# Kernel optimization log

Measured on AMD Instinct MI355X. Metric: run time of the kernel, lower is better.

Reference implementation:

```python
import jax, jax.numpy as jnp
import numpy as np

B, L, H, F, K, NBINS, T = 32, 512, 512, 512, 3, 256, 4096
EPS = 1e-8  # RMSNorm epsilon
PAD = (K - 1) // 2  # =1, matches both conv paddings in the torch module


def _conv1d(x, w, b):
    # x: [B, L, Cin], w: [K, Cin, Cout]
    return jax.lax.conv_general_dilated(
        x, w, window_strides=(1,), padding=[(PAD, PAD)],
        dimension_numbers=('NLC', 'LIO', 'NLC')) + b


def _rms(x, g):
    return g * x / (jnp.sqrt(jnp.mean(x * x, axis=-1, keepdims=True)) + EPS)


def _vpred(x, mask, w1, b1, g1, w2, b2, g2, wl, bl):
    h = _rms(jax.nn.relu(_conv1d(x, w1, b1)), g1)
    h = _rms(jax.nn.relu(_conv1d(h, w2, b2)), g2)
    out = (h @ wl + bl)[..., 0]  # [B, L]
    return jnp.where(mask, 0.0, out)


def _proj(x, w1, b1, w2, b2):
    return jax.nn.relu(jax.nn.relu(x @ w1 + b1) @ w2 + b2)


def _length_regulate(x, dur, max_len):
    # Vectorized equivalent of LengthRegulator: repeat phoneme i dur[b,i] times, pad to max_len.
    cum = jnp.cumsum(dur, axis=1)               # [B, L]
    mel_len = cum[:, -1]                        # [B]
    t = jnp.arange(max_len)                     # [T]
    idx = jax.vmap(lambda c: jnp.searchsorted(c, t, side='right'))(cum)  # [B, T]
    idx = jnp.minimum(idx, x.shape[1] - 1)
    out = jnp.take_along_axis(x, idx[:, :, None], axis=1)  # [B, T, H]
    valid = (t[None, :] < mel_len[:, None])
    return out * valid[:, :, None].astype(x.dtype), mel_len


def setup_inputs() -> dict:
    key = jax.random.key(0)
    ks = iter(jax.random.split(key, 64))
    n = lambda *s: jax.random.normal(next(ks), s, jnp.float32) * 0.05
    inp = {}
    inp['x'] = jax.random.normal(next(ks), (B, L, H), jnp.float32)
    inp['embedding'] = jax.random.normal(next(ks), (B, L, H), jnp.float32)
    inp['src_mask'] = jnp.zeros((B, L), bool)
    inp['duration_target'] = jax.random.randint(next(ks), (B, L), 0, 9, jnp.int32)
    inp['pitch_target'] = jax.random.normal(next(ks), (B, L), jnp.float32)
    inp['energy_target'] = jax.random.normal(next(ks), (B, L), jnp.float32)
    inp['max_len'] = T
    for p in ['dur', 'pit', 'eng']:
        inp[p + '_w1'] = n(K, H, F); inp[p + '_b1'] = jnp.zeros(F, jnp.float32)
        inp[p + '_g1'] = jnp.ones(F, jnp.float32)
        inp[p + '_w2'] = n(K, F, F); inp[p + '_b2'] = jnp.zeros(F, jnp.float32)
        inp[p + '_g2'] = jnp.ones(F, jnp.float32)
        inp[p + '_wl'] = n(F, 1); inp[p + '_bl'] = jnp.zeros(1, jnp.float32)
    for p in ['pp', 'ep', 'sp']:
        inp[p + '_w1'] = n(H, H); inp[p + '_b1'] = jnp.zeros(H, jnp.float32)
        inp[p + '_w2'] = n(H, H); inp[p + '_b2'] = jnp.zeros(H, jnp.float32)
    inp['pitch_bins'] = jnp.linspace(-3.0, 3.0, NBINS - 1)
    inp['energy_bins'] = jnp.linspace(-3.0, 3.0, NBINS - 1)
    inp['pitch_emb'] = n(NBINS, H)
    inp['energy_emb'] = n(NBINS, H)
    return inp


def reference(x, embedding, src_mask, duration_target, pitch_target, energy_target, max_len,
              dur_w1, dur_b1, dur_g1, dur_w2, dur_b2, dur_g2, dur_wl, dur_bl,
              pit_w1, pit_b1, pit_g1, pit_w2, pit_b2, pit_g2, pit_wl, pit_bl,
              eng_w1, eng_b1, eng_g1, eng_w2, eng_b2, eng_g2, eng_wl, eng_bl,
              pp_w1, pp_b1, pp_w2, pp_b2,
              ep_w1, ep_b1, ep_w2, ep_b2,
              sp_w1, sp_b1, sp_w2, sp_b2,
              pitch_bins, energy_bins, pitch_emb, energy_emb):
    log_dur = _vpred(x, src_mask, dur_w1, dur_b1, dur_g1, dur_w2, dur_b2, dur_g2, dur_wl, dur_bl)
    pit_pred = _vpred(x + _proj(embedding, pp_w1, pp_b1, pp_w2, pp_b2), src_mask,
                      pit_w1, pit_b1, pit_g1, pit_w2, pit_b2, pit_g2, pit_wl, pit_bl)
    pitch_embedding = pitch_emb[jnp.searchsorted(pitch_bins, pitch_target)]  # torch.bucketize right=False == side='left'
    eng_pred = _vpred(x + _proj(embedding, ep_w1, ep_b1, ep_w2, ep_b2), src_mask,
                      eng_w1, eng_b1, eng_g1, eng_w2, eng_b2, eng_g2, eng_wl, eng_bl)
    energy_embedding = energy_emb[jnp.searchsorted(energy_bins, energy_target)]
    xo = x + energy_embedding + pitch_embedding + _proj(embedding, sp_w1, sp_b1, sp_w2, sp_b2)
    out, mel_len = _length_regulate(xo, duration_target, max_len)
    return (out, pit_pred, eng_pred, log_dur, mel_len)
```

## Files before the change

### kernel.cpp

```cpp
#include <hip/hip_runtime.h>

#define Bv    32
#define Lv    512
#define Hv    512
#define Fv    512
#define Tv    4096
#define Mv    (Bv*Lv)
#define NBINSv 256

#define OUT_OFF 0
#define PIT_OFF (Bv*(size_t)Tv*Hv)
#define ENG_OFF (PIT_OFF + Mv)
#define DUR_OFF (ENG_OFF + Mv)
#define MEL_OFF (DUR_OFF + Mv)

typedef unsigned short ushort;
typedef __attribute__((ext_vector_type(8))) short   bf16x8;
typedef __attribute__((ext_vector_type(4))) float   f32x4;
typedef __attribute__((ext_vector_type(8))) unsigned short u16x8;

__device__ __forceinline__ float b2f(ushort u) {
    union { float f; unsigned u; } x; x.u = ((unsigned)u) << 16; return x.f;
}
__device__ __forceinline__ ushort f2b(float f) {
    union { float f; unsigned u; } x; x.f = f;
    unsigned r = x.u + 0x7fffu + ((x.u >> 16) & 1u);
    return (ushort)(r >> 16);
}

#define GLL16(g, l) __builtin_amdgcn_global_load_lds( \
    (const __attribute__((address_space(1))) void*)(g), \
    (__attribute__((address_space(3))) void*)(l), 16, 0, 0)

template<int NZ> struct GArgs {
    const ushort* A[NZ];
    const ushort* W[NZ];
    const float*  bias[NZ];
    ushort*       C[NZ];
};
struct RmsArgs   { const ushort* h[3]; const float* g[3]; ushort* o[3]; };
struct RlArgs    { const ushort* h[3]; const float* g[3]; const float* wl[3]; const float* bl[3]; };
struct TransArgs { const float* src[6]; ushort* dst[6]; };
struct ConvArgs  { const float* src[2]; ushort* dst[2]; };

template<int NTAPS, int EPI, int NZ>
__global__ __launch_bounds__(256) void gemm_bf16_kernel(
    GArgs<NZ> ga, const float* __restrict__ res, const float* __restrict__ pe,
    const float* __restrict__ ee, const int* __restrict__ idxp,
    const int* __restrict__ idxe, const ushort* __restrict__ zp)
{
    constexpr int KTOT = NTAPS * 512;
    const int z = (NZ > 1) ? blockIdx.z : 0;
    const ushort* __restrict__ A    = ga.A[z];
    const ushort* __restrict__ Bt   = ga.W[z];
    const float*  __restrict__ bias = ga.bias[z];
    ushort*       __restrict__ C    = ga.C[z];

    __shared__ ushort As[128 * 32];
    __shared__ ushort Bs[128 * 32];

    const int tid = threadIdx.x;
    const int n0 = blockIdx.x * 128;
    const int m0 = blockIdx.y * 128;

    const int sar = tid >> 2;
    const int sl  = tid & 3;

    const int lane = tid & 63;
    const int w    = tid >> 6;
    const int wm   = (w & 1) * 64;
    const int wn   = (w >> 1) * 64;
    const int lr   = lane & 15;
    const int q    = lane >> 4;

    ushort* asd0 = &As[sar * 32 + sl * 8];
    ushort* asd1 = &As[(sar + 64) * 32 + sl * 8];
    ushort* bsd0 = &Bs[sar * 32 + sl * 8];
    ushort* bsd1 = &Bs[(sar + 64) * 32 + sl * 8];

    f32x4 acc[4][4];
    #pragma unroll
    for (int j = 0; j < 4; ++j)
        #pragma unroll
        for (int i = 0; i < 4; ++i) {
            f32x4 zz = {0.f, 0.f, 0.f, 0.f};
            acc[j][i] = zz;
        }

    for (int tap = 0; tap < NTAPS; ++tap) {
        const ushort* ab[2];
        #pragma unroll
        for (int r = 0; r < 2; ++r) {
            const int row = sar + r * 64;
            const int m   = m0 + row;
            if (NTAPS == 3) {
                const int l  = m & (Lv - 1);
                const int ls = l + tap - 1;
                ab[r] = ((unsigned)ls < (unsigned)Lv)
                      ? A + (size_t)(m + tap - 1) * 512 + sl * 8 : nullptr;
            } else {
                ab[r] = A + (size_t)m * 512 + sl * 8;
            }
        }
        const ushort* bb0 = Bt + (size_t)(n0 + sar) * KTOT + tap * 512 + sl * 8;
        const ushort* bb1 = Bt + (size_t)(n0 + sar + 64) * KTOT + tap * 512 + sl * 8;

        for (int kt = 0; kt < 16; ++kt) {
            const int kin = kt << 5;
            GLL16(ab[0] ? ab[0] + kin : zp, asd0);
            GLL16(bb0 + kin, bsd0);
            GLL16(ab[1] ? ab[1] + kin : zp, asd1);
            GLL16(bb1 + kin, bsd1);
            __syncthreads();

            bf16x8 af[4], bfr[4];
            #pragma unroll
            for (int i = 0; i < 4; ++i) {
                af[i]  = *(const bf16x8*)&As[(wm + i * 16 + lr) * 32 + q * 8];
                bfr[i] = *(const bf16x8*)&Bs[(wn + i * 16 + lr) * 32 + q * 8];
            }
            #pragma unroll
            for (int j = 0; j < 4; ++j)
                #pragma unroll
                for (int i = 0; i < 4; ++i)
                    acc[j][i] = __builtin_amdgcn_mfma_f32_16x16x32_bf16(
                                    bfr[j], af[i], acc[j][i], 0, 0, 0);
            __syncthreads();
        }
    }

    #pragma unroll
    for (int i = 0; i < 4; ++i) {
        const int m = m0 + wm + i * 16 + lr;
        const size_t ro = (size_t)m * 512;
        int ip = 0, ie = 0;
        if (EPI == 2) { ip = idxp[m]; ie = idxe[m]; }
        #pragma unroll
        for (int j = 0; j < 4; ++j) {
            const int n = n0 + wn + j * 16 + q * 4;
            const f32x4 a = acc[j][i];
            const float4 bi = *(const float4*)(bias + n);
            float v0 = fmaxf(a[0] + bi.x, 0.f);
            float v1 = fmaxf(a[1] + bi.y, 0.f);
            float v2 = fmaxf(a[2] + bi.z, 0.f);
            float v3 = fmaxf(a[3] + bi.w, 0.f);
            if (EPI >= 1) {
                const float4 r4 = *(const float4*)(res + ro + n);
                v0 += r4.x; v1 += r4.y; v2 += r4.z; v3 += r4.w;
            }
            if (EPI == 2) {
                const float4 p4 = *(const float4*)(pe + (size_t)ip * 512 + n);
                const float4 e4 = *(const float4*)(ee + (size_t)ie * 512 + n);
                v0 += p4.x + e4.x; v1 += p4.y + e4.y;
                v2 += p4.z + e4.z; v3 += p4.w + e4.w;
            }
            ushort4 o4;
            o4.x = f2b(v0); o4.y = f2b(v1); o4.z = f2b(v2); o4.w = f2b(v3);
            *(ushort4*)(C + ro + n) = o4;
        }
    }
}

__global__ __launch_bounds__(256) void convert_kernel(ConvArgs ca)
{
    const float* __restrict__ X  = ca.src[blockIdx.y];
    ushort*      __restrict__ Xb = ca.dst[blockIdx.y];
    const size_t i = (size_t)blockIdx.x * 256 + threadIdx.x;
    const float4 a = ((const float4*)X)[2 * i];
    const float4 b = ((const float4*)X)[2 * i + 1];
    u16x8 o;
    o[0] = f2b(a.x); o[1] = f2b(a.y); o[2] = f2b(a.z); o[3] = f2b(a.w);
    o[4] = f2b(b.x); o[5] = f2b(b.y); o[6] = f2b(b.z); o[7] = f2b(b.w);
    *(u16x8*)(Xb + i * 8) = o;
}

__global__ __launch_bounds__(256) void transpose_kernel(TransArgs ta, int Ktot)
{
    const float* __restrict__ W  = ta.src[blockIdx.z];
    ushort*      __restrict__ Wt = ta.dst[blockIdx.z];
    __shared__ float t[32][33];
    const int k0 = blockIdx.x * 32, n0 = blockIdx.y * 32;
    const int r = threadIdx.x >> 5, c = threadIdx.x & 31;
    #pragma unroll
    for (int rr = 0; rr < 4; ++rr)
        t[r + rr * 8][c] = W[(size_t)(k0 + r + rr * 8) * 512 + n0 + c];
    __syncthreads();
    #pragma unroll
    for (int rr = 0; rr < 4; ++rr)
        Wt[(size_t)(n0 + r + rr * 8) * Ktot + k0 + c] = f2b(t[c][r + rr * 8]);
}

__global__ __launch_bounds__(128) void rms_kernel(RmsArgs ra)
{
    const int z = blockIdx.y;
    const int row = blockIdx.x;
    const int tid = threadIdx.x;
    const ushort* __restrict__ h = ra.h[z];
    const ushort4 hv = ((const ushort4*)(h + (size_t)row * 512))[tid];
    const float v0 = b2f(hv.x), v1 = b2f(hv.y), v2 = b2f(hv.z), v3 = b2f(hv.w);
    float ss = v0 * v0 + v1 * v1 + v2 * v2 + v3 * v3;
    #pragma unroll
    for (int off = 32; off; off >>= 1) ss += __shfl_down(ss, off, 64);
    __shared__ float p[2];
    if ((tid & 63) == 0) p[tid >> 6] = ss;
    __syncthreads();
    const float tot = p[0] + p[1];
    const float inv = 1.f / (sqrtf(tot * (1.f / 512.f)) + 1e-8f);
    const float4 gv = ((const float4*)ra.g[z])[tid];
    ushort4 ov;
    ov.x = f2b(gv.x * v0 * inv); ov.y = f2b(gv.y * v1 * inv);
    ov.z = f2b(gv.z * v2 * inv); ov.w = f2b(gv.w * v3 * inv);
    ((ushort4*)(ra.o[z] + (size_t)row * 512))[tid] = ov;
}

__global__ __launch_bounds__(256) void rmslin_kernel(
    RlArgs ra, const unsigned char* __restrict__ mask, float* __restrict__ predbase)
{
    const int z = blockIdx.y;
    const int wave = threadIdx.x >> 6, lane = threadIdx.x & 63;
    const int row = blockIdx.x * 4 + wave;
    const ushort* __restrict__ h = ra.h[z];
    const bf16x8 hv = *(const bf16x8*)(h + (size_t)row * 512 + lane * 8);
    const float4 g0 = *(const float4*)(ra.g[z] + lane * 8);
    const float4 g1 = *(const float4*)(ra.g[z] + lane * 8 + 4);
    const float4 w0 = *(const float4*)(ra.wl[z] + lane * 8);
    const float4 w1 = *(const float4*)(ra.wl[z] + lane * 8 + 4);
    float hf[8];
    #pragma unroll
    for (int t = 0; t < 8; ++t) hf[t] = b2f((ushort)hv[t]);
    float ss = 0.f, sgw = 0.f;
    #pragma unroll
    for (int t = 0; t < 8; ++t) ss += hf[t] * hf[t];
    sgw += hf[0]*g0.x*w0.x + hf[1]*g0.y*w0.y + hf[2]*g0.z*w0.z + hf[3]*g0.w*w0.w;
    sgw += hf[4]*g1.x*w1.x + hf[5]*g1.y*w1.y + hf[6]*g1.z*w1.z + hf[7]*g1.w*w1.w;
    #pragma unroll
    for (int off = 32; off; off >>= 1) {
        ss  += __shfl_down(ss,  off, 64);
        sgw += __shfl_down(sgw, off, 64);
    }
    if (lane == 0) {
        const float inv = 1.f / (sqrtf(ss * (1.f / 512.f)) + 1e-8f);
        predbase[(size_t)z * Mv + row] = mask[row] ? 0.f : (sgw * inv + ra.bl[z][0]);
    }
}

__global__ __launch_bounds__(256) void idx_kernel(
    const float* __restrict__ pt, const float* __restrict__ et,
    const float* __restrict__ pbins, const float* __restrict__ ebins,
    int* __restrict__ idxp, int* __restrict__ idxe)
{
    __shared__ float pb[NBINSv - 1], ebn[NBINSv - 1];
    const int tid = threadIdx.x;
    if (tid < NBINSv - 1) { pb[tid] = pbins[tid]; ebn[tid] = ebins[tid]; }
    __syncthreads();
    const int m = blockIdx.x * 256 + tid;
    const float pv = pt[m], ev = et[m];
    int lo = 0, hi = NBINSv - 1;
    while (lo < hi) { int mid = (lo + hi) >> 1; if (pb[mid] < pv) lo = mid + 1; else hi = mid; }
    idxp[m] = lo;
    lo = 0; hi = NBINSv - 1;
    while (lo < hi) { int mid = (lo + hi) >> 1; if (ebn[mid] < ev) lo = mid + 1; else hi = mid; }
    idxe[m] = lo;
}

__global__ __launch_bounds__(512) void cumtmap_kernel(
    const int* __restrict__ dur, float* __restrict__ melout, int* __restrict__ tmap)
{
    __shared__ int s[Lv];
    const int b = blockIdx.x, tid = threadIdx.x;
    s[tid] = dur[b * Lv + tid];
    __syncthreads();
    for (int off = 1; off < Lv; off <<= 1) {
        int t = (tid >= off) ? s[tid - off] : 0;
        __syncthreads();
        s[tid] += t;
        __syncthreads();
    }
    const int mel = s[Lv - 1];
    if (tid == 0) melout[b] = (float)mel;
    #pragma unroll
    for (int rr = 0; rr < Tv / 512; ++rr) {
        const int t = tid + rr * 512;
        int lo = 0, hi = Lv;
        while (lo < hi) { int mid = (lo + hi) >> 1; if (s[mid] <= t) lo = mid + 1; else hi = mid; }
        tmap[b * Tv + t] = (t < mel) ? (b * Lv + min(lo, Lv - 1)) : -1;
    }
}

__global__ __launch_bounds__(128) void regulate_kernel(
    const ushort* __restrict__ xo, const int* __restrict__ tmap,
    float* __restrict__ out)
{
    const int bt = blockIdx.x;
    const int src = tmap[bt];
    float4 v = make_float4(0.f, 0.f, 0.f, 0.f);
    if (src >= 0) {
        const ushort4 u = ((const ushort4*)(xo + (size_t)src * 512))[threadIdx.x];
        v.x = b2f(u.x); v.y = b2f(u.y); v.z = b2f(u.z); v.w = b2f(u.w);
    }
    ((float4*)(out + (size_t)bt * 512))[threadIdx.x] = v;
}

extern "C" void kernel_launch(void* const* d_in, const int* in_sizes, int n_in,
                              void* d_out, int out_size, void* d_ws, size_t ws_size,
                              hipStream_t stream)
{
    const float* x    = (const float*)d_in[0];
    const float* emb  = (const float*)d_in[1];
    const unsigned char* mask = (const unsigned char*)d_in[2];
    const int*   durt = (const int*)d_in[3];
    const float* pt   = (const float*)d_in[4];
    const float* et   = (const float*)d_in[5];
    const float* dw1 = (const float*)d_in[7],  *db1 = (const float*)d_in[8],
               * dg1 = (const float*)d_in[9],  *dw2 = (const float*)d_in[10],
               * db2 = (const float*)d_in[11], *dg2 = (const float*)d_in[12],
               * dwl = (const float*)d_in[13], *dbl = (const float*)d_in[14];
    const float* pw1 = (const float*)d_in[15], *pb1 = (const float*)d_in[16],
               * pg1 = (const float*)d_in[17], *pw2 = (const float*)d_in[18],
               * pb2 = (const float*)d_in[19], *pg2 = (const float*)d_in[20],
               * pwl = (const float*)d_in[21], *pbl = (const float*)d_in[22];
    const float* ew1 = (const float*)d_in[23], *eb1 = (const float*)d_in[24],
               * eg1 = (const float*)d_in[25], *ew2 = (const float*)d_in[26],
               * eb2 = (const float*)d_in[27], *eg2 = (const float*)d_in[28],
               * ewl = (const float*)d_in[29], *ebl = (const float*)d_in[30];
    const float* ppw1 = (const float*)d_in[31], *ppb1 = (const float*)d_in[32],
               * ppw2 = (const float*)d_in[33], *ppb2 = (const float*)d_in[34];
    const float* epw1 = (const float*)d_in[35], *epb1 = (const float*)d_in[36],
               * epw2 = (const float*)d_in[37], *epb2 = (const float*)d_in[38];
    const float* spw1 = (const float*)d_in[39], *spb1 = (const float*)d_in[40],
               * spw2 = (const float*)d_in[41], *spb2 = (const float*)d_in[42];
    const float* pbins = (const float*)d_in[43];
    const float* ebins = (const float*)d_in[44];
    const float* pemb  = (const float*)d_in[45];
    const float* eemb  = (const float*)d_in[46];

    float* outf = (float*)d_out;

    int*    idxp   = (int*)d_ws;
    int*    idxe   = idxp + 16384;
    ushort* zp     = (ushort*)(idxe + 16384);
    int*    tmap   = idxe + 16448;
    ushort* xob    = (ushort*)((float*)d_ws + 262144);

    #define OBUF(i) ((ushort*)(outf + (size_t)(i) * 4194304))
    ushort* xb  = OBUF(0);   ushort* eb  = OBUF(1);
    ushort* pA0 = OBUF(2);   ushort* pA1 = OBUF(3);  ushort* pA2 = OBUF(4);
    ushort* xp  = OBUF(5);   ushort* xe  = OBUF(6);
    ushort* c0  = OBUF(7);   ushort* c1  = OBUF(8);  ushort* c2  = OBUF(9);
    ushort* r0  = OBUF(10);  ushort* r1  = OBUF(11); ushort* r2  = OBUF(12);
    ushort* wt[12];
    {
        size_t off = 13ull * 4194304;
        for (int i = 0; i < 6; ++i)  { wt[i] = (ushort*)(outf + off); off += 393216; }
        for (int i = 6; i < 12; ++i) { wt[i] = (ushort*)(outf + off); off += 131072; }
    }

    hipMemsetAsync(zp, 0, 64, stream);

    { ConvArgs ca = {{x, emb}, {xb, eb}};
      convert_kernel<<<dim3(4096, 2), 256, 0, stream>>>(ca); }
    { TransArgs ta = {{dw1, dw2, pw1, pw2, ew1, ew2}, {wt[0], wt[1], wt[2], wt[3], wt[4], wt[5]}};
      transpose_kernel<<<dim3(48, 16, 6), 256, 0, stream>>>(ta, 1536); }
    { TransArgs ta = {{ppw1, ppw2, epw1, epw2, spw1, spw2},
                      {wt[6], wt[7], wt[8], wt[9], wt[10], wt[11]}};
      transpose_kernel<<<dim3(16, 16, 6), 256, 0, stream>>>(ta, 512); }

    idx_kernel<<<Mv / 256, 256, 0, stream>>>(pt, et, pbins, ebins, idxp, idxe);
    cumtmap_kernel<<<Bv, Lv, 0, stream>>>(durt, outf + MEL_OFF, tmap);

    const dim3 g3(Fv / 128, Mv / 128, 3);
    const dim3 g2(Fv / 128, Mv / 128, 2);
    const dim3 g1(Fv / 128, Mv / 128, 1);

    { GArgs<3> a = {{eb, eb, eb}, {wt[6], wt[8], wt[10]}, {ppb1, epb1, spb1}, {pA0, pA1, pA2}};
      gemm_bf16_kernel<1, 0, 3><<<g3, 256, 0, stream>>>(a, nullptr, nullptr, nullptr,
                                                        nullptr, nullptr, zp); }
    { GArgs<2> a = {{pA0, pA1}, {wt[7], wt[9]}, {ppb2, epb2}, {xp, xe}};
      gemm_bf16_kernel<1, 1, 2><<<g2, 256, 0, stream>>>(a, x, nullptr, nullptr,
                                                        nullptr, nullptr, zp); }
    { GArgs<1> a = {{pA2}, {wt[11]}, {spb2}, {xob}};
      gemm_bf16_kernel<1, 2, 1><<<g1, 256, 0, stream>>>(a, x, pemb, eemb, idxp, idxe, zp); }

    { GArgs<3> a = {{xp, xe, xb}, {wt[2], wt[4], wt[0]}, {pb1, eb1, db1}, {c0, c1, c2}};
      gemm_bf16_kernel<3, 0, 3><<<g3, 256, 0, stream>>>(a, nullptr, nullptr, nullptr,
                                                        nullptr, nullptr, zp); }
    { RmsArgs ra = {{c0, c1, c2}, {pg1, eg1, dg1}, {r0, r1, r2}};
      rms_kernel<<<dim3(Mv, 3), 128, 0, stream>>>(ra); }
    { GArgs<3> a = {{r0, r1, r2}, {wt[3], wt[5], wt[1]}, {pb2, eb2, db2}, {c0, c1, c2}};
      gemm_bf16_kernel<3, 0, 3><<<g3, 256, 0, stream>>>(a, nullptr, nullptr, nullptr,
                                                        nullptr, nullptr, zp); }
    { RlArgs ra = {{c0, c1, c2}, {pg2, eg2, dg2}, {pwl, ewl, dwl}, {pbl, ebl, dbl}};
      rmslin_kernel<<<dim3(Mv / 4, 3), 256, 0, stream>>>(ra, mask, outf + PIT_OFF); }

    regulate_kernel<<<Bv * Tv, 128, 0, stream>>>(xob, tmap, outf + OUT_OFF);
}
```

Measured before the change: 880.7 us.

## Double-buffer GEMM LDS tiles, swizzle LDS layout, merge second projection GEMMs

The bf16 GEMM now double-buffers its A/B tiles in shared memory. The load for the next k-step is issued before computing the current one, with a single barrier per iteration, and the tap loop is flattened into one k loop. The LDS column chunks are rotated by row (a swizzle on both the global-load source and the fragment read) to reduce bank conflicts. The epilogue mode becomes a per-z runtime field, so the two second-stage projection GEMMs (EPI 1 and EPI 2) merge into one 3-way launch. In exchange, shared memory per block doubles and the epilogue carries runtime branches.

Result: no change. 868.9 us (-1.3%).

```diff
diff --git a/kernel.cpp b/kernel.cpp
--- a/kernel.cpp
+++ b/kernel.cpp
@@ -37,27 +37,30 @@
     const ushort* W[NZ];
     const float*  bias[NZ];
     ushort*       C[NZ];
+    int           epi[NZ];
 };
 struct RmsArgs   { const ushort* h[3]; const float* g[3]; ushort* o[3]; };
 struct RlArgs    { const ushort* h[3]; const float* g[3]; const float* wl[3]; const float* bl[3]; };
 struct TransArgs { const float* src[6]; ushort* dst[6]; };
 struct ConvArgs  { const float* src[2]; ushort* dst[2]; };
 
-template<int NTAPS, int EPI, int NZ>
+template<int NTAPS, int NZ>
 __global__ __launch_bounds__(256) void gemm_bf16_kernel(
     GArgs<NZ> ga, const float* __restrict__ res, const float* __restrict__ pe,
     const float* __restrict__ ee, const int* __restrict__ idxp,
     const int* __restrict__ idxe, const ushort* __restrict__ zp)
 {
     constexpr int KTOT = NTAPS * 512;
+    constexpr int KT   = NTAPS * 16;
     const int z = (NZ > 1) ? blockIdx.z : 0;
     const ushort* __restrict__ A    = ga.A[z];
     const ushort* __restrict__ Bt   = ga.W[z];
     const float*  __restrict__ bias = ga.bias[z];
     ushort*       __restrict__ C    = ga.C[z];
-
-    __shared__ ushort As[128 * 32];
-    __shared__ ushort Bs[128 * 32];
+    const int em = ga.epi[z];
+
+    __shared__ ushort As[2][128 * 32];
+    __shared__ ushort Bs[2][128 * 32];
 
     const int tid = threadIdx.x;
     const int n0 = blockIdx.x * 128;
@@ -65,6 +68,7 @@
 
     const int sar = tid >> 2;
     const int sl  = tid & 3;
+    const int qg  = ((sl - (sar >> 1)) & 3) << 3;
 
     const int lane = tid & 63;
     const int w    = tid >> 6;
@@ -72,11 +76,38 @@
     const int wn   = (w >> 1) * 64;
     const int lr   = lane & 15;
     const int q    = lane >> 4;
-
-    ushort* asd0 = &As[sar * 32 + sl * 8];
-    ushort* asd1 = &As[(sar + 64) * 32 + sl * 8];
-    ushort* bsd0 = &Bs[sar * 32 + sl * 8];
-    ushort* bsd1 = &Bs[(sar + 64) * 32 + sl * 8];
+    const int slot = ((q + (lr >> 1)) & 3) << 3;
+
+    ushort* ad[2][2];
+    ushort* bd[2][2];
+    #pragma unroll
+    for (int b = 0; b < 2; ++b) {
+        ad[b][0] = &As[b][sar * 32 + sl * 8];
+        ad[b][1] = &As[b][(sar + 64) * 32 + sl * 8];
+        bd[b][0] = &Bs[b][sar * 32 + sl * 8];
+        bd[b][1] = &Bs[b][(sar + 64) * 32 + sl * 8];
+    }
+
+    auto stage = [&](int kt, int buf) {
+        const int tap = (NTAPS == 3) ? (kt >> 4) : 0;
+        const int kin = (kt & 15) << 5;
+        #pragma unroll
+        for (int r = 0; r < 2; ++r) {
+            const int row = sar + r * 64;
+            const int m   = m0 + row;
+            const ushort* asrc;
+            if (NTAPS == 3) {
+                const int ls = (m & (Lv - 1)) + tap - 1;
+                asrc = ((unsigned)ls < (unsigned)Lv)
+                     ? A + (size_t)(m + tap - 1) * 512 + kin + qg : zp;
+            } else {
+                asrc = A + (size_t)m * 512 + kin + qg;
+            }
+            GLL16(asrc, ad[buf][r]);
+            const ushort* bsrc = Bt + (size_t)(n0 + row) * KTOT + tap * 512 + kin + qg;
+            GLL16(bsrc, bd[buf][r]);
+        }
+    };
 
     f32x4 acc[4][4];
     #pragma unroll
@@ -87,46 +118,24 @@
             acc[j][i] = zz;
         }
 
-    for (int tap = 0; tap < NTAPS; ++tap) {
-        const ushort* ab[2];
+    stage(0, 0);
+    for (int kt = 0; kt < KT; ++kt) {
+        const int cur = kt & 1;
+        __syncthreads();
+        if (kt + 1 < KT) stage(kt + 1, cur ^ 1);
+
+        bf16x8 af[4], bfr[4];
         #pragma unroll
-        for (int r = 0; r < 2; ++r) {
-            const int row = sar + r * 64;
-            const int m   = m0 + row;
-            if (NTAPS == 3) {
-                const int l  = m & (Lv - 1);
-                const int ls = l + tap - 1;
-                ab[r] = ((unsigned)ls < (unsigned)Lv)
-                      ? A + (size_t)(m + tap - 1) * 512 + sl * 8 : nullptr;
-            } else {
-                ab[r] = A + (size_t)m * 512 + sl * 8;
-            }
+        for (int i = 0; i < 4; ++i) {
+            af[i]  = *(const bf16x8*)&As[cur][(wm + i * 16 + lr) * 32 + slot];
+            bfr[i] = *(const bf16x8*)&Bs[cur][(wn + i * 16 + lr) * 32 + slot];
         }
-        const ushort* bb0 = Bt + (size_t)(n0 + sar) * KTOT + tap * 512 + sl * 8;
-        const ushort* bb1 = Bt + (size_t)(n0 + sar + 64) * KTOT + tap * 512 + sl * 8;
-
-        for (int kt = 0; kt < 16; ++kt) {
-            const int kin = kt << 5;
-            GLL16(ab[0] ? ab[0] + kin : zp, asd0);
-            GLL16(bb0 + kin, bsd0);
-            GLL16(ab[1] ? ab[1] + kin : zp, asd1);
-            GLL16(bb1 + kin, bsd1);
-            __syncthreads();
-
-            bf16x8 af[4], bfr[4];
+        #pragma unroll
+        for (int j = 0; j < 4; ++j)
             #pragma unroll
-            for (int i = 0; i < 4; ++i) {
-                af[i]  = *(const bf16x8*)&As[(wm + i * 16 + lr) * 32 + q * 8];
-                bfr[i] = *(const bf16x8*)&Bs[(wn + i * 16 + lr) * 32 + q * 8];
-            }
-            #pragma unroll
-            for (int j = 0; j < 4; ++j)
-                #pragma unroll
-                for (int i = 0; i < 4; ++i)
-                    acc[j][i] = __builtin_amdgcn_mfma_f32_16x16x32_bf16(
-                                    bfr[j], af[i], acc[j][i], 0, 0, 0);
-            __syncthreads();
-        }
+            for (int i = 0; i < 4; ++i)
+                acc[j][i] = __builtin_amdgcn_mfma_f32_16x16x32_bf16(
+                                bfr[j], af[i], acc[j][i], 0, 0, 0);
     }
 
     #pragma unroll
@@ -134,7 +143,7 @@
         const int m = m0 + wm + i * 16 + lr;
         const size_t ro = (size_t)m * 512;
         int ip = 0, ie = 0;
-        if (EPI == 2) { ip = idxp[m]; ie = idxe[m]; }
+        if (em == 2) { ip = idxp[m]; ie = idxe[m]; }
         #pragma unroll
         for (int j = 0; j < 4; ++j) {
             const int n = n0 + wn + j * 16 + q * 4;
@@ -144,11 +153,11 @@
             float v1 = fmaxf(a[1] + bi.y, 0.f);
             float v2 = fmaxf(a[2] + bi.z, 0.f);
             float v3 = fmaxf(a[3] + bi.w, 0.f);
-            if (EPI >= 1) {
+            if (em >= 1) {
                 const float4 r4 = *(const float4*)(res + ro + n);
                 v0 += r4.x; v1 += r4.y; v2 += r4.z; v3 += r4.w;
             }
-            if (EPI == 2) {
+            if (em == 2) {
                 const float4 p4 = *(const float4*)(pe + (size_t)ip * 512 + n);
                 const float4 e4 = *(const float4*)(ee + (size_t)ie * 512 + n);
                 v0 += p4.x + e4.x; v1 += p4.y + e4.y;
@@ -369,26 +378,25 @@
     cumtmap_kernel<<<Bv, Lv, 0, stream>>>(durt, outf + MEL_OFF, tmap);
 
     const dim3 g3(Fv / 128, Mv / 128, 3);
-    const dim3 g2(Fv / 128, Mv / 128, 2);
-    const dim3 g1(Fv / 128, Mv / 128, 1);
-
-    { GArgs<3> a = {{eb, eb, eb}, {wt[6], wt[8], wt[10]}, {ppb1, epb1, spb1}, {pA0, pA1, pA2}};
-      gemm_bf16_kernel<1, 0, 3><<<g3, 256, 0, stream>>>(a, nullptr, nullptr, nullptr,
-                                                        nullptr, nullptr, zp); }
-    { GArgs<2> a = {{pA0, pA1}, {wt[7], wt[9]}, {ppb2, epb2}, {xp, xe}};
-      gemm_bf16_kernel<1, 1, 2><<<g2, 256, 0, stream>>>(a, x, nullptr, nullptr,
-                                                        nullptr, nullptr, zp); }
-    { GArgs<1> a = {{pA2}, {wt[11]}, {spb2}, {xob}};
-      gemm_bf16_kernel<1, 2, 1><<<g1, 256, 0, stream>>>(a, x, pemb, eemb, idxp, idxe, zp); }
-
-    { GArgs<3> a = {{xp, xe, xb}, {wt[2], wt[4], wt[0]}, {pb1, eb1, db1}, {c0, c1, c2}};
-      gemm_bf16_kernel<3, 0, 3><<<g3, 256, 0, stream>>>(a, nullptr, nullptr, nullptr,
-                                                        nullptr, nullptr, zp); }
+
+    { GArgs<3> a = {{eb, eb, eb}, {wt[6], wt[8], wt[10]}, {ppb1, epb1, spb1},
+                    {pA0, pA1, pA2}, {0, 0, 0}};
+      gemm_bf16_kernel<1, 3><<<g3, 256, 0, stream>>>(a, nullptr, nullptr, nullptr,
+                                                     nullptr, nullptr, zp); }
+    { GArgs<3> a = {{pA0, pA1, pA2}, {wt[7], wt[9], wt[11]}, {ppb2, epb2, spb2},
+                    {xp, xe, xob}, {1, 1, 2}};
+      gemm_bf16_kernel<1, 3><<<g3, 256, 0, stream>>>(a, x, pemb, eemb, idxp, idxe, zp); }
+
+    { GArgs<3> a = {{xp, xe, xb}, {wt[2], wt[4], wt[0]}, {pb1, eb1, db1},
+                    {c0, c1, c2}, {0, 0, 0}};
+      gemm_bf16_kernel<3, 3><<<g3, 256, 0, stream>>>(a, nullptr, nullptr, nullptr,
+                                                     nullptr, nullptr, zp); }
     { RmsArgs ra = {{c0, c1, c2}, {pg1, eg1, dg1}, {r0, r1, r2}};
       rms_kernel<<<dim3(Mv, 3), 128, 0, stream>>>(ra); }
-    { GArgs<3> a = {{r0, r1, r2}, {wt[3], wt[5], wt[1]}, {pb2, eb2, db2}, {c0, c1, c2}};
-      gemm_bf16_kernel<3, 0, 3><<<g3, 256, 0, stream>>>(a, nullptr, nullptr, nullptr,
-                                                        nullptr, nullptr, zp); }
+    { GArgs<3> a = {{r0, r1, r2}, {wt[3], wt[5], wt[1]}, {pb2, eb2, db2},
+                    {c0, c1, c2}, {0, 0, 0}};
+      gemm_bf16_kernel<3, 3><<<g3, 256, 0, stream>>>(a, nullptr, nullptr, nullptr,
+                                                     nullptr, nullptr, zp); }
     { RlArgs ra = {{c0, c1, c2}, {pg2, eg2, dg2}, {pwl, ewl, dwl}, {pbl, ebl, dbl}};
       rmslin_kernel<<<dim3(Mv / 4, 3), 256, 0, stream>>>(ra, mask, outf + PIT_OFF); }
 
```
